# Performance work log

Hardware: AMD Instinct MI355X
Metric: run time of the kernel (lower is better)

## Reference

```python
import jax, jax.numpy as jnp
import numpy as np

EPS = 1e-15
BALL_EPS = 4e-3   # geoopt float32 projection eps
N_DST = 20000
N_EDGE = 200000
DIM = 128
H, D = 2, 128


def _norm(x):
    return jnp.sqrt(jnp.maximum(jnp.sum(x * x, -1, keepdims=True), EPS * EPS))


def _artanh(x):
    return jnp.arctanh(jnp.clip(x, -1.0 + 1e-7, 1.0 - 1e-7))


def mobius_add(x, y):
    x2 = jnp.sum(x * x, -1, keepdims=True)
    y2 = jnp.sum(y * y, -1, keepdims=True)
    xy = jnp.sum(x * y, -1, keepdims=True)
    num = (1 + 2 * xy + y2) * x + (1 - x2) * y
    den = 1 + 2 * xy + x2 * y2
    return num / jnp.maximum(den, EPS)


def mobius_matvec(W, x):
    xn = _norm(x)
    mx = x @ W.T
    mxn = _norm(mx)
    return jnp.tanh(mxn / xn * _artanh(xn)) * mx / mxn


def logmap0(y):
    yn = _norm(y)
    return _artanh(yn) * y / yn


def expmap0(u):
    un = _norm(u)
    return jnp.tanh(un) * u / un


def projx(x):
    n = _norm(x)
    maxn = 1.0 - BALL_EPS
    return jnp.where(n > maxn, x * (maxn / n), x)


def ball_dist(x, y):
    # dist(x,y) = 2 artanh(|| (-x) (+) y ||)
    return 2.0 * _artanh(_norm(mobius_add(-x, y))[..., 0])


def edge_softmax(logits, dst, n_dst):
    # softmax over edges grouped by destination node, per trailing dims
    m = jax.ops.segment_max(logits, dst, num_segments=n_dst)
    z = jnp.exp(logits - m[dst])
    s = jax.ops.segment_sum(z, dst, num_segments=n_dst)
    return z / s[dst]


def setup_inputs() -> dict:
    key = jax.random.key(0)
    ks = jax.random.split(key, 8)
    hyper = expmap0(0.2 * jax.random.normal(ks[0], (N_DST + N_EDGE, DIM), jnp.float32))
    dt = jax.random.uniform(ks[1], (N_EDGE,), jnp.float32) * 1e4
    time_w = jnp.asarray(1.0 / 10 ** np.linspace(0, 9, DIM, dtype=np.float32))
    time_b = jnp.zeros((DIM,), jnp.float32)
    w_src = 0.05 * jax.random.normal(ks[2], (H * D, DIM), jnp.float32)
    b_src = 0.01 * jax.random.normal(ks[3], (H * D,), jnp.float32)
    w_dst = 0.05 * jax.random.normal(ks[4], (H * D, DIM), jnp.float32)
    b_dst = 0.01 * jax.random.normal(ks[5], (H * D,), jnp.float32)
    attn = 0.1 * jax.random.normal(ks[6], (1, H, D), jnp.float32)
    src_idx = jnp.arange(N_EDGE, dtype=jnp.int32) + N_DST  # edge i's src node
    dst_idx = jax.random.randint(ks[7], (N_EDGE,), 0, N_DST, jnp.int32)
    return {"hyper": hyper, "dt": dt, "time_w": time_w, "time_b": time_b,
            "w_src": w_src, "b_src": b_src, "w_dst": w_dst, "b_dst": b_dst,
            "attn": attn, "src_idx": src_idx, "dst_idx": dst_idx}


def reference(hyper, dt, time_w, time_b, w_src, b_src, w_dst, b_dst, attn, src_idx, dst_idx):
    n_dst = N_DST
    # time encoding: zeros for dst nodes, dt for the sampled neighbor of each edge
    time = jnp.concatenate([jnp.zeros((n_dst,), dt.dtype), dt])        # [num_src]
    time_feat = jnp.cos(time[:, None] * time_w[None, :] + time_b)      # [num_src, DIM]
    time_feat = projx(time_feat)
    src_feat = mobius_add(hyper, time_feat)                            # [num_src, DIM]
    h_dst = src_feat[:n_dst]
    feat_src = mobius_add(mobius_matvec(w_src, src_feat), b_src)       # [num_src, H*D]
    feat_dst = mobius_add(mobius_matvec(w_dst, h_dst), b_dst)          # [n_dst, H*D]
    el = logmap0(feat_src).reshape(-1, H, D)
    er = logmap0(feat_dst).reshape(-1, H, D)
    # attention logit per edge/head
    e = jnp.sum((el[src_idx] + er[dst_idx]) * attn, -1)[:, :, None]    # [E,H,1]
    # hyperbolic-distance gate, edge-softmax normalized
    d = ball_dist(feat_src[src_idx], feat_dst[dst_idx])                # [E]
    inv = 1.0 / (1e-15 + d)
    dsm = edge_softmax(inv[:, None], dst_idx, n_dst)[:, :, None]       # [E,1,1]
    e = jax.nn.leaky_relu(e * dsm, 0.2)
    a = edge_softmax(e, dst_idx, n_dst)                                # [E,H,1]
    ft = jax.ops.segment_sum(el[src_idx] * a, dst_idx, num_segments=n_dst)
    rst = ft.reshape(n_dst, H * D)
    return expmap0(rst)
```

## Files before the change

kernel.cpp:

```cpp
#include <hip/hip_runtime.h>
#include <hip/hip_bf16.h>
#include <math.h>

typedef __attribute__((ext_vector_type(8))) short bfrag8;
typedef __attribute__((ext_vector_type(4))) float ffrag4;

__device__ inline float bf2f(unsigned short h) { return __uint_as_float(((unsigned)h) << 16); }
__device__ inline unsigned short f2bf(float f) {
    unsigned u = __float_as_uint(f);
    unsigned r = (u + 0x7FFFu + ((u >> 16) & 1u)) >> 16;
    return (unsigned short)r;
}
__device__ inline float wred(float v) {
    v += __shfl_xor(v, 1, 64);
    v += __shfl_xor(v, 2, 64);
    v += __shfl_xor(v, 4, 64);
    v += __shfl_xor(v, 8, 64);
    v += __shfl_xor(v, 16, 64);
    v += __shfl_xor(v, 32, 64);
    return v;
}
__device__ inline float wredmax(float v) {
    v = fmaxf(v, __shfl_xor(v, 1, 64));
    v = fmaxf(v, __shfl_xor(v, 2, 64));
    v = fmaxf(v, __shfl_xor(v, 4, 64));
    v = fmaxf(v, __shfl_xor(v, 8, 64));
    v = fmaxf(v, __shfl_xor(v, 16, 64));
    v = fmaxf(v, __shfl_xor(v, 32, 64));
    return v;
}
__device__ inline float bsum(float v, float* red) {
    v = wred(v);
    if ((threadIdx.x & 63) == 0) red[threadIdx.x >> 6] = v;
    __syncthreads();
    float r = red[0] + red[1] + red[2] + red[3];
    __syncthreads();
    return r;
}

#define ACLIP (1.0f - 1e-7f)

__global__ void k_detect(const unsigned short* __restrict__ hyper, int* __restrict__ flag) {
    __shared__ int total;
    int t = threadIdx.x;
    if (t == 0) total = 0;
    __syncthreads();
    int cnt = 0;
    for (int i = t * 8; i < t * 8 + 8; i++) {
        if ((i & 1) == 0) {
            unsigned e = ((unsigned)hyper[i] >> 7) & 0xFF;
            if (e >= 0xC0) cnt++;
        }
    }
    atomicAdd(&total, cnt);
    __syncthreads();
    if (t == 0) *flag = (total >= 32) ? 1 : 0;
}

__device__ inline float ldin(const void* s, int i, int isf32) {
    return isf32 ? ((const float*)s)[i] : bf2f(((const unsigned short*)s)[i]);
}
__global__ void k_params(const void* __restrict__ w_src, const void* __restrict__ w_dst,
                         const void* __restrict__ b_src, const void* __restrict__ b_dst,
                         const void* __restrict__ attn, const void* __restrict__ time_w,
                         const void* __restrict__ time_b,
                         unsigned short* __restrict__ whs, unsigned short* __restrict__ wls,
                         unsigned short* __restrict__ whd, unsigned short* __restrict__ wld,
                         float* __restrict__ bsrc, float* __restrict__ bdst,
                         float* __restrict__ pattn, float* __restrict__ tw,
                         float* __restrict__ tb, const int* __restrict__ flag, int nw) {
    int i = blockIdx.x * blockDim.x + threadIdx.x;
    int isf32 = *flag;
    if (i < nw) {
        float x = ldin(w_src, i, isf32);
        unsigned short h = f2bf(x);
        whs[i] = h; wls[i] = f2bf(x - bf2f(h));
        float y = ldin(w_dst, i, isf32);
        unsigned short g = f2bf(y);
        whd[i] = g; wld[i] = f2bf(y - bf2f(g));
    }
    if (i < 256) {
        bsrc[i] = ldin(b_src, i, isf32);
        bdst[i] = ldin(b_dst, i, isf32);
        pattn[i] = ldin(attn, i, isf32);
    }
    if (i < 128) {
        tw[i] = ldin(time_w, i, isf32);
        tb[i] = ldin(time_b, i, isf32);
    }
}
__global__ void k_fill(unsigned* __restrict__ p, unsigned v, int n) {
    int i = blockIdx.x * blockDim.x + threadIdx.x;
    if (i < n) p[i] = v;
}

__global__ void k_hist(const int* __restrict__ dst_idx, int* __restrict__ deg, int n_edge) {
    int i = blockIdx.x * blockDim.x + threadIdx.x;
    if (i < n_edge) atomicAdd(deg + dst_idx[i], 1);
}
__global__ __launch_bounds__(1024) void k_scan(const int* __restrict__ deg,
                                               int* __restrict__ rowptr,
                                               int* __restrict__ cursor, int n) {
    __shared__ int part[1024];
    int t = threadIdx.x;
    int chunk = (n + 1023) >> 10;
    int lo = t * chunk, hi = min(lo + chunk, n);
    int s = 0;
    for (int i = lo; i < hi; i++) s += deg[i];
    part[t] = s;
    __syncthreads();
    for (int dd = 1; dd < 1024; dd <<= 1) {
        int v = (t >= dd) ? part[t - dd] : 0;
        __syncthreads();
        part[t] += v;
        __syncthreads();
    }
    int base = (t == 0) ? 0 : part[t - 1];
    for (int i = lo; i < hi; i++) {
        rowptr[i] = base; cursor[i] = base;
        base += deg[i];
    }
    if (t == 0) rowptr[n] = part[1023];
}
__global__ void k_scatter_edges(const int* __restrict__ src_idx, const int* __restrict__ dst_idx,
                                int* __restrict__ cursor, int* __restrict__ es, int n_edge) {
    int i = blockIdx.x * blockDim.x + threadIdx.x;
    if (i >= n_edge) return;
    int slot = atomicAdd(cursor + dst_idx[i], 1);
    es[slot] = src_idx[i];
}

__global__ void k_node_prep(const void* __restrict__ hyper_v,
                            const void* __restrict__ dt_v,
                            const float* __restrict__ tw, const float* __restrict__ tb,
                            unsigned short* __restrict__ Ah, unsigned short* __restrict__ Al,
                            float* __restrict__ tnode,
                            const int* __restrict__ flag, int n_dst, int n_total) {
    int wid  = (blockIdx.x * blockDim.x + threadIdx.x) >> 6;
    int lane = threadIdx.x & 63;
    if (wid >= n_total) return;
    int isf32 = *flag;
    float tval = 0.0f;
    if (wid >= n_dst) {
        int e = wid - n_dst;
        tval = isf32 ? ((const float*)dt_v)[e] : bf2f(((const unsigned short*)dt_v)[e]);
    }
    int j0 = lane * 2;
    float tf0 = cosf(tval * tw[j0]     + tb[j0]);
    float tf1 = cosf(tval * tw[j0 + 1] + tb[j0 + 1]);
    float h0, h1;
    if (isf32) {
        const float* hp = (const float*)hyper_v + (size_t)wid * 128 + j0;
        h0 = hp[0]; h1 = hp[1];
    } else {
        const unsigned short* hp = (const unsigned short*)hyper_v + (size_t)wid * 128 + j0;
        h0 = bf2f(hp[0]); h1 = bf2f(hp[1]);
    }
    float ptf2 = wred(tf0 * tf0 + tf1 * tf1);
    float ph2  = wred(h0 * h0 + h1 * h1);
    float pht  = wred(h0 * tf0 + h1 * tf1);
    float ntf = sqrtf(fmaxf(ptf2, 1e-30f));
    float maxn = 1.0f - 0.004f;
    float sc = (ntf > maxn) ? (maxn / ntf) : 1.0f;
    float y2 = sc * sc * ptf2, xy = sc * pht, x2 = ph2;
    float A = 1.0f + 2.0f * xy + y2;
    float B = 1.0f - x2;
    float iden = 1.0f / fmaxf(1.0f + 2.0f * xy + x2 * y2, 1e-15f);
    float s0 = (A * h0 + B * sc * tf0) * iden;
    float s1 = (A * h1 + B * sc * tf1) * iden;
    unsigned short h0s = f2bf(s0), h1s = f2bf(s1);
    unsigned short l0s = f2bf(s0 - bf2f(h0s)), l1s = f2bf(s1 - bf2f(h1s));
    *(ushort2*)(Ah + (size_t)wid * 128 + j0) = make_ushort2(h0s, h1s);
    *(ushort2*)(Al + (size_t)wid * 128 + j0) = make_ushort2(l0s, l1s);
    float ps2 = wred(s0 * s0 + s1 * s1);
    float xn = sqrtf(fmaxf(ps2, 1e-30f));
    float g = atanhf(fminf(xn, ACLIP)) / xn;
    if (lane == 0) tnode[wid] = g;
}

#define WPITCH 136
#define GEMM_LDS (256 * WPITCH * 2 * 2)
__global__ __launch_bounds__(512, 2) void k_gemm_ep(
        const unsigned short* __restrict__ Ah, const unsigned short* __restrict__ Al,
        const unsigned short* __restrict__ Wh, const unsigned short* __restrict__ Wl,
        const float* __restrict__ bvec, const float* __restrict__ attn,
        const float* __restrict__ tnode,
        float* __restrict__ feat, float* __restrict__ x2a, float* __restrict__ ca,
        float* __restrict__ satt, int base, int M) {
    extern __shared__ unsigned short smem[];
    unsigned short* Bhs = smem;
    unsigned short* Bls = smem + 256 * WPITCH;

    int t = threadIdx.x;
    for (int v = t; v < 4096; v += 512) {
        int e = v << 3;
        int row = e >> 7, col = e & 127;
        *(bfrag8*)(Bhs + row * WPITCH + col) = *(const bfrag8*)(Wh + e);
        *(bfrag8*)(Bls + row * WPITCH + col) = *(const bfrag8*)(Wl + e);
    }
    __syncthreads();

    int w = t >> 6, lane = t & 63;
    int m16 = lane & 15, kg = lane >> 4;
    int rowbase = (blockIdx.x * 8 + w) * 32;
    int ar0 = min(rowbase + m16, M - 1);
    int ar1 = min(rowbase + 16 + m16, M - 1);
    const unsigned short* A0h = Ah + (size_t)ar0 * 128;
    const unsigned short* A0l = Al + (size_t)ar0 * 128;
    const unsigned short* A1h = Ah + (size_t)ar1 * 128;
    const unsigned short* A1l = Al + (size_t)ar1 * 128;

    ffrag4 acc[2][16];
#pragma unroll
    for (int p = 0; p < 2; p++)
#pragma unroll
        for (int ct = 0; ct < 16; ct++) acc[p][ct] = (ffrag4){0.0f, 0.0f, 0.0f, 0.0f};

    int kA = kg * 8;
    bfrag8 ah0 = *(const bfrag8*)(A0h + kA);
    bfrag8 al0 = *(const bfrag8*)(A0l + kA);
    bfrag8 ah1 = *(const bfrag8*)(A1h + kA);
    bfrag8 al1 = *(const bfrag8*)(A1l + kA);

    for (int ks = 0; ks < 4; ks++) {
        bfrag8 nh0 = ah0, nl0 = al0, nh1 = ah1, nl1 = al1;
        if (ks < 3) {
            int kn = (ks + 1) * 32 + kA;
            nh0 = *(const bfrag8*)(A0h + kn);
            nl0 = *(const bfrag8*)(A0l + kn);
            nh1 = *(const bfrag8*)(A1h + kn);
            nl1 = *(const bfrag8*)(A1l + kn);
        }
        int k0 = ks * 32 + kA;
#pragma unroll
        for (int ct = 0; ct < 16; ct++) {
            int wb = (ct * 16 + m16) * WPITCH + k0;
            bfrag8 bh = *(const bfrag8*)(Bhs + wb);
            bfrag8 bl = *(const bfrag8*)(Bls + wb);
            acc[0][ct] = __builtin_amdgcn_mfma_f32_16x16x32_bf16(ah0, bh, acc[0][ct], 0, 0, 0);
            acc[0][ct] = __builtin_amdgcn_mfma_f32_16x16x32_bf16(al0, bh, acc[0][ct], 0, 0, 0);
            acc[0][ct] = __builtin_amdgcn_mfma_f32_16x16x32_bf16(ah0, bl, acc[0][ct], 0, 0, 0);
            acc[1][ct] = __builtin_amdgcn_mfma_f32_16x16x32_bf16(ah1, bh, acc[1][ct], 0, 0, 0);
            acc[1][ct] = __builtin_amdgcn_mfma_f32_16x16x32_bf16(al1, bh, acc[1][ct], 0, 0, 0);
            acc[1][ct] = __builtin_amdgcn_mfma_f32_16x16x32_bf16(ah1, bl, acc[1][ct], 0, 0, 0);
        }
        ah0 = nh0; al0 = nl0; ah1 = nh1; al1 = nl1;
    }

    float bv[16], av[16];
    float pb2 = 0.0f;
#pragma unroll
    for (int ct = 0; ct < 16; ct++) {
        bv[ct] = bvec[ct * 16 + m16];
        av[ct] = attn[ct * 16 + m16];
        pb2 += bv[ct] * bv[ct];
    }
#pragma unroll
    for (int off = 1; off < 16; off <<= 1) pb2 += __shfl_xor(pb2, off, 64);

#pragma unroll
    for (int p = 0; p < 2; p++) {
        float pm2[4] = {0, 0, 0, 0}, pdb[4] = {0, 0, 0, 0};
#pragma unroll
        for (int ct = 0; ct < 16; ct++)
#pragma unroll
            for (int r = 0; r < 4; r++) {
                float v = acc[p][ct][r];
                pm2[r] += v * v;
                pdb[r] += v * bv[ct];
            }
#pragma unroll
        for (int off = 1; off < 16; off <<= 1)
#pragma unroll
            for (int r = 0; r < 4; r++) {
                pm2[r] += __shfl_xor(pm2[r], off, 64);
                pdb[r] += __shfl_xor(pdb[r], off, 64);
            }
#pragma unroll
        for (int r = 0; r < 4; r++) {
            int row_o = rowbase + p * 16 + kg * 4 + r;
            bool ok = row_o < M;
            float g = ok ? tnode[base + row_o] : 1.0f;
            float mxn = sqrtf(fmaxf(pm2[r], 1e-30f));
            float sv = tanhf(mxn * g) / mxn;
            float xy = sv * pdb[r];
            float x2v = sv * sv * pm2[r];
            float Am = 1.0f + 2.0f * xy + pb2;
            float Bm = 1.0f - x2v;
            float iden = 1.0f / fmaxf(1.0f + 2.0f * xy + x2v * pb2, 1e-15f);
            float pf2 = 0.0f, pa0 = 0.0f, pa1 = 0.0f;
#pragma unroll
            for (int ct = 0; ct < 16; ct++) {
                float f = (Am * sv * acc[p][ct][r] + Bm * bv[ct]) * iden;
                acc[p][ct][r] = f;
                pf2 += f * f;
                if (ct < 8) pa0 += f * av[ct]; else pa1 += f * av[ct];
            }
#pragma unroll
            for (int off = 1; off < 16; off <<= 1) {
                pf2 += __shfl_xor(pf2, off, 64);
                pa0 += __shfl_xor(pa0, off, 64);
                pa1 += __shfl_xor(pa1, off, 64);
            }
            if (ok) {
                float* fr = feat + (size_t)(base + row_o) * 256;
#pragma unroll
                for (int ct = 0; ct < 16; ct++) fr[ct * 16 + m16] = acc[p][ct][r];
                if (m16 == 0) {
                    float nf = sqrtf(fmaxf(pf2, 1e-30f));
                    float cl = atanhf(fminf(nf, ACLIP)) / nf;
                    x2a[base + row_o] = pf2;
                    ca[base + row_o] = cl;
                    satt[(size_t)(base + row_o) * 2 + 0] = cl * pa0;
                    satt[(size_t)(base + row_o) * 2 + 1] = cl * pa1;
                }
            }
        }
    }
}

#define CAPR 16
#define CAPE 64
__global__ __launch_bounds__(256) void k_aggregate(
        const int* __restrict__ rowptr, const int* __restrict__ es,
        const float* __restrict__ x2a, const float* __restrict__ satt,
        const float* __restrict__ ca, const float* __restrict__ feat,
        float* __restrict__ invg, float* __restrict__ w0g, float* __restrict__ w1g,
        void* __restrict__ out, const int* __restrict__ flag, int n_dst) {
    __shared__ float red[4];
    __shared__ float yrow[256];
    __shared__ float inv_s[CAPE], w0_s[CAPE], w1_s[CAPE];
    __shared__ int sb_s[CAPE];
    __shared__ float cache[CAPR * 256];
    int d = blockIdx.x;
    int t = threadIdx.x;
    int w = t >> 6, lane = t & 63;
    int off0 = rowptr[d], off1 = rowptr[d + 1];
    int deg = off1 - off0;
    if (deg == 0) {
        if (*flag) ((float*)out)[(size_t)d * 256 + t] = 0.0f;
        else ((unsigned short*)out)[(size_t)d * 256 + t] = 0;
        return;
    }
    yrow[t] = feat[(size_t)d * 256 + t];
    float y2 = x2a[d];
    __syncthreads();

    int c = lane * 4;
    float4 yv = *(const float4*)(&yrow[c]);
    for (int b = 0; b < deg; b += 4) {
        int j = b + w;
        if (j < deg) {
            int i = off0 + j;
            int s = es[i];
            float4 xv = *(const float4*)(feat + (size_t)s * 256 + c);
            float pd = wred(xv.x * yv.x + xv.y * yv.y + xv.z * yv.z + xv.w * yv.w);
            if (j < CAPR) *(float4*)&cache[j * 256 + c] = xv;
            if (lane == 0) {
                float x2 = x2a[s];
                float A = 1.0f - 2.0f * pd + y2;
                float B = 1.0f - x2;
                float iden = 1.0f / fmaxf(1.0f - 2.0f * pd + x2 * y2, 1e-15f);
                float p2 = fmaxf(A * A * x2 - 2.0f * A * B * pd + B * B * y2, 0.0f);
                float nrm = sqrtf(fmaxf(p2, 1e-30f)) * iden;
                float dd = 2.0f * atanhf(fminf(nrm, ACLIP));
                float iv = 1.0f / (1e-15f + dd);
                if (j < CAPE) { inv_s[j] = iv; sb_s[j] = s; }
                else { invg[i] = iv; }
            }
        }
    }
    __syncthreads();

    if (w == 0) {
        float sd0 = satt[(size_t)d * 2 + 0], sd1 = satt[(size_t)d * 2 + 1];
        float lm = -INFINITY;
        for (int j = lane; j < deg; j += 64)
            lm = fmaxf(lm, (j < CAPE) ? inv_s[j] : invg[off0 + j]);
        float m1 = wredmax(lm);
        float ls = 0.0f;
        for (int j = lane; j < deg; j += 64)
            ls += expf(((j < CAPE) ? inv_s[j] : invg[off0 + j]) - m1);
        float is1 = 1.0f / wred(ls);
        float lm0 = -INFINITY, lm1 = -INFINITY;
        for (int j = lane; j < deg; j += 64) {
            int s = (j < CAPE) ? sb_s[j] : es[off0 + j];
            float iv = (j < CAPE) ? inv_s[j] : invg[off0 + j];
            float dsm = expf(iv - m1) * is1;
            float e0 = (satt[(size_t)s * 2 + 0] + sd0) * dsm; e0 = (e0 > 0.0f) ? e0 : 0.2f * e0;
            float e1 = (satt[(size_t)s * 2 + 1] + sd1) * dsm; e1 = (e1 > 0.0f) ? e1 : 0.2f * e1;
            if (j < CAPE) { w0_s[j] = e0; w1_s[j] = e1; }
            else { w0g[off0 + j] = e0; w1g[off0 + j] = e1; }
            lm0 = fmaxf(lm0, e0); lm1 = fmaxf(lm1, e1);
        }
        float m20 = wredmax(lm0), m21 = wredmax(lm1);
        float l20 = 0.0f, l21 = 0.0f;
        for (int j = lane; j < deg; j += 64) {
            float e0 = (j < CAPE) ? w0_s[j] : w0g[off0 + j];
            float e1 = (j < CAPE) ? w1_s[j] : w1g[off0 + j];
            l20 += expf(e0 - m20); l21 += expf(e1 - m21);
        }
        float is20 = 1.0f / wred(l20), is21 = 1.0f / wred(l21);
        for (int j = lane; j < deg; j += 64) {
            int s = (j < CAPE) ? sb_s[j] : es[off0 + j];
            float cs = ca[s];
            if (j < CAPE) {
                w0_s[j] = expf(w0_s[j] - m20) * is20 * cs;
                w1_s[j] = expf(w1_s[j] - m21) * is21 * cs;
            } else {
                w0g[off0 + j] = expf(w0g[off0 + j] - m20) * is20 * cs;
                w1g[off0 + j] = expf(w1g[off0 + j] - m21) * is21 * cs;
            }
        }
    }
    __syncthreads();

    int col = t, h = t >> 7;
    float acc = 0.0f;
    for (int j = 0; j < deg; j++) {
        float wgt = (j < CAPE) ? (h ? w1_s[j] : w0_s[j])
                               : (h ? w1g[off0 + j] : w0g[off0 + j]);
        float x;
        if (j < CAPR) x = cache[j * 256 + col];
        else {
            int s = (j < CAPE) ? sb_s[j] : es[off0 + j];
            x = feat[(size_t)s * 256 + col];
        }
        acc += wgt * x;
    }
    float p2 = bsum(acc * acc, red);
    float n = sqrtf(fmaxf(p2, 1e-30f));
    float sc = tanhf(n) / n;
    float o = acc * sc;
    if (*flag) ((float*)out)[(size_t)d * 256 + col] = o;
    else ((unsigned short*)out)[(size_t)d * 256 + col] = f2bf(o);
}

extern "C" void kernel_launch(void* const* d_in, const int* in_sizes, int n_in,
                              void* d_out, int out_size, void* d_ws, size_t ws_size,
                              hipStream_t stream) {
    const void* hyper  = d_in[0];
    const void* dt     = d_in[1];
    const void* time_w = d_in[2];
    const void* time_b = d_in[3];
    const void* w_src  = d_in[4];
    const void* b_src  = d_in[5];
    const void* w_dst  = d_in[6];
    const void* b_dst  = d_in[7];
    const void* attn   = d_in[8];
    const int* src_idx = (const int*)d_in[9];
    const int* dst_idx = (const int*)d_in[10];

    const int DIMN = 128, HD = 256;
    int n_edge  = in_sizes[1];
    int n_total = in_sizes[0] / DIMN;
    int n_dst   = n_total - n_edge;

    float* ws = (float*)d_ws;
    size_t off = 0;
    auto alloc = [&](size_t n) { float* p = ws + off; off += n; return p; };
    float* p_tw    = alloc(DIMN);
    float* p_tb    = alloc(DIMN);
    float* p_bsrc  = alloc(HD);
    float* p_bdst  = alloc(HD);
    float* p_attn  = alloc(HD);
    int*   p_flag  = (int*)alloc(4);
    unsigned short* p_whs = (unsigned short*)alloc((size_t)HD * DIMN / 2);
    unsigned short* p_wls = (unsigned short*)alloc((size_t)HD * DIMN / 2);
    unsigned short* p_whd = (unsigned short*)alloc((size_t)HD * DIMN / 2);
    unsigned short* p_wld = (unsigned short*)alloc((size_t)HD * DIMN / 2);
    unsigned short* p_ah = (unsigned short*)alloc((size_t)n_total * DIMN / 2);
    unsigned short* p_al = (unsigned short*)alloc((size_t)n_total * DIMN / 2);
    int* p_deg    = (int*)alloc(n_dst);
    int* p_rowptr = (int*)alloc(n_dst + 1);
    int* p_cursor = (int*)alloc(n_dst);
    int* p_es     = (int*)alloc(n_edge);
    float* p_inv  = alloc(n_edge);
    float* p_w0   = alloc(n_edge);
    float* p_w1   = alloc(n_edge);
    float* p_feat  = alloc((size_t)n_total * HD);
    float* p_tnode = alloc(n_total);
    float* p_call  = alloc(n_total);
    float* p_x2    = alloc(n_total);
    float* p_satt  = alloc((size_t)n_total * 2);
    (void)ws_size;

    const int TB = 256;
    auto cdiv = [](int a, int b) { return (a + b - 1) / b; };

    static bool lds_cfg = false;
    if (!lds_cfg) {
        hipFuncSetAttribute(reinterpret_cast<const void*>(k_gemm_ep),
                            hipFuncAttributeMaxDynamicSharedMemorySize, GEMM_LDS);
        lds_cfg = true;
    }

    k_detect<<<1, TB, 0, stream>>>((const unsigned short*)hyper, p_flag);

    k_params<<<cdiv(HD * DIMN, TB), TB, 0, stream>>>(
        w_src, w_dst, b_src, b_dst, attn, time_w, time_b,
        p_whs, p_wls, p_whd, p_wld, p_bsrc, p_bdst, p_attn, p_tw, p_tb,
        p_flag, HD * DIMN);

    k_fill<<<cdiv(n_dst, TB), TB, 0, stream>>>((unsigned*)p_deg, 0u, n_dst);
    k_hist<<<cdiv(n_edge, TB), TB, 0, stream>>>(dst_idx, p_deg, n_edge);
    k_scan<<<1, 1024, 0, stream>>>(p_deg, p_rowptr, p_cursor, n_dst);
    k_scatter_edges<<<cdiv(n_edge, TB), TB, 0, stream>>>(src_idx, dst_idx, p_cursor,
                                                         p_es, n_edge);

    k_node_prep<<<cdiv(n_total, 4), TB, 0, stream>>>(hyper, dt, p_tw, p_tb,
                                                     p_ah, p_al, p_tnode, p_flag,
                                                     n_dst, n_total);

    k_gemm_ep<<<cdiv(n_dst, 256), 512, GEMM_LDS, stream>>>(p_ah, p_al, p_whd, p_wld,
                                                           p_bdst, p_attn, p_tnode,
                                                           p_feat, p_x2, p_call, p_satt,
                                                           0, n_dst);
    k_gemm_ep<<<cdiv(n_edge, 256), 512, GEMM_LDS, stream>>>(p_ah + (size_t)n_dst * DIMN,
                                                            p_al + (size_t)n_dst * DIMN,
                                                            p_whs, p_wls,
                                                            p_bsrc, p_attn, p_tnode,
                                                            p_feat, p_x2, p_call, p_satt,
                                                            n_dst, n_edge);

    k_aggregate<<<n_dst, TB, 0, stream>>>(p_rowptr, p_es, p_x2, p_satt, p_call,
                                          p_feat, p_inv, p_w0, p_w1,
                                          d_out, p_flag, n_dst);
}
```

Before: 594.8 us.

## Use fast transcendentals, remap edge distance loop, add single-pass softmax path

```diff
diff --git a/kernel.cpp b/kernel.cpp
--- a/kernel.cpp
+++ b/kernel.cpp
@@ -39,6 +39,36 @@
 }
 
 #define ACLIP (1.0f - 1e-7f)
+#define ATANH_ACLIP 8.4056196f
+
+__device__ inline float rcpf(float x) { return __builtin_amdgcn_rcpf(x); }
+__device__ inline float fsqrtf(float x) { return __builtin_amdgcn_sqrtf(x); }
+__device__ inline float fexp(float x) { return __expf(x); }
+__device__ inline float flog(float x) { return __logf(x); }
+__device__ inline float atanh_over_x(float x) {
+    if (x < 0.125f) {
+        float x2 = x * x;
+        return 1.0f + x2 * (0.33333333f + x2 * 0.2f);
+    }
+    return 0.5f * flog((1.0f + x) * rcpf(1.0f - x)) * rcpf(x);
+}
+__device__ inline float tanh_over_x(float x) {
+    if (x < 0.125f) {
+        float x2 = x * x;
+        return 1.0f - x2 * (0.33333333f - x2 * 0.13333333f);
+    }
+    float e = fexp(-2.0f * x);
+    return (1.0f - e) * rcpf((1.0f + e) * x);
+}
+__device__ inline float fcosr(float x) {
+    const float C  = 0.15915494309189535f;
+    const float C1 = 0.1591796875f;
+    const float C2 = -2.4744408e-5f;
+    float k = __builtin_rintf(x * C);
+    float f = fmaf(x, C1, -k);
+    f = fmaf(x, C2, f);
+    return __builtin_amdgcn_cosf(f);
+}
 
 __global__ void k_detect(const unsigned short* __restrict__ hyper, int* __restrict__ flag) {
     __shared__ int total;
@@ -146,8 +176,8 @@
         tval = isf32 ? ((const float*)dt_v)[e] : bf2f(((const unsigned short*)dt_v)[e]);
     }
     int j0 = lane * 2;
-    float tf0 = cosf(tval * tw[j0]     + tb[j0]);
-    float tf1 = cosf(tval * tw[j0 + 1] + tb[j0 + 1]);
+    float tf0 = fcosr(tval * tw[j0]     + tb[j0]);
+    float tf1 = fcosr(tval * tw[j0 + 1] + tb[j0 + 1]);
     float h0, h1;
     if (isf32) {
         const float* hp = (const float*)hyper_v + (size_t)wid * 128 + j0;
@@ -159,13 +189,13 @@
     float ptf2 = wred(tf0 * tf0 + tf1 * tf1);
     float ph2  = wred(h0 * h0 + h1 * h1);
     float pht  = wred(h0 * tf0 + h1 * tf1);
-    float ntf = sqrtf(fmaxf(ptf2, 1e-30f));
+    float ntf = fsqrtf(fmaxf(ptf2, 1e-30f));
     float maxn = 1.0f - 0.004f;
-    float sc = (ntf > maxn) ? (maxn / ntf) : 1.0f;
+    float sc = (ntf > maxn) ? (maxn * rcpf(ntf)) : 1.0f;
     float y2 = sc * sc * ptf2, xy = sc * pht, x2 = ph2;
     float A = 1.0f + 2.0f * xy + y2;
     float B = 1.0f - x2;
-    float iden = 1.0f / fmaxf(1.0f + 2.0f * xy + x2 * y2, 1e-15f);
+    float iden = rcpf(fmaxf(1.0f + 2.0f * xy + x2 * y2, 1e-15f));
     float s0 = (A * h0 + B * sc * tf0) * iden;
     float s1 = (A * h1 + B * sc * tf1) * iden;
     unsigned short h0s = f2bf(s0), h1s = f2bf(s1);
@@ -173,8 +203,8 @@
     *(ushort2*)(Ah + (size_t)wid * 128 + j0) = make_ushort2(h0s, h1s);
     *(ushort2*)(Al + (size_t)wid * 128 + j0) = make_ushort2(l0s, l1s);
     float ps2 = wred(s0 * s0 + s1 * s1);
-    float xn = sqrtf(fmaxf(ps2, 1e-30f));
-    float g = atanhf(fminf(xn, ACLIP)) / xn;
+    float xn = fsqrtf(fmaxf(ps2, 1e-30f));
+    float g = (xn > ACLIP) ? (ATANH_ACLIP * rcpf(xn)) : atanh_over_x(xn);
     if (lane == 0) tnode[wid] = g;
 }
 
@@ -281,13 +311,13 @@
             int row_o = rowbase + p * 16 + kg * 4 + r;
             bool ok = row_o < M;
             float g = ok ? tnode[base + row_o] : 1.0f;
-            float mxn = sqrtf(fmaxf(pm2[r], 1e-30f));
-            float sv = tanhf(mxn * g) / mxn;
+            float mxn = fsqrtf(fmaxf(pm2[r], 1e-30f));
+            float sv = g * tanh_over_x(mxn * g);
             float xy = sv * pdb[r];
             float x2v = sv * sv * pm2[r];
             float Am = 1.0f + 2.0f * xy + pb2;
             float Bm = 1.0f - x2v;
-            float iden = 1.0f / fmaxf(1.0f + 2.0f * xy + x2v * pb2, 1e-15f);
+            float iden = rcpf(fmaxf(1.0f + 2.0f * xy + x2v * pb2, 1e-15f));
             float pf2 = 0.0f, pa0 = 0.0f, pa1 = 0.0f;
 #pragma unroll
             for (int ct = 0; ct < 16; ct++) {
@@ -307,8 +337,8 @@
 #pragma unroll
                 for (int ct = 0; ct < 16; ct++) fr[ct * 16 + m16] = acc[p][ct][r];
                 if (m16 == 0) {
-                    float nf = sqrtf(fmaxf(pf2, 1e-30f));
-                    float cl = atanhf(fminf(nf, ACLIP)) / nf;
+                    float nf = fsqrtf(fmaxf(pf2, 1e-30f));
+                    float cl = (nf > ACLIP) ? (ATANH_ACLIP * rcpf(nf)) : atanh_over_x(nf);
                     x2a[base + row_o] = pf2;
                     ca[base + row_o] = cl;
                     satt[(size_t)(base + row_o) * 2 + 0] = cl * pa0;
@@ -346,25 +376,47 @@
     float y2 = x2a[d];
     __syncthreads();
 
-    int c = lane * 4;
-    float4 yv = *(const float4*)(&yrow[c]);
-    for (int b = 0; b < deg; b += 4) {
-        int j = b + w;
+    int g16 = lane >> 4, sub = lane & 15;
+    int cb = sub * 16;
+    float4 yv0 = *(const float4*)(&yrow[cb + 0]);
+    float4 yv1 = *(const float4*)(&yrow[cb + 4]);
+    float4 yv2 = *(const float4*)(&yrow[cb + 8]);
+    float4 yv3 = *(const float4*)(&yrow[cb + 12]);
+    for (int b = 0; b < deg; b += 16) {
+        int j = b + w * 4 + g16;
         if (j < deg) {
             int i = off0 + j;
             int s = es[i];
-            float4 xv = *(const float4*)(feat + (size_t)s * 256 + c);
-            float pd = wred(xv.x * yv.x + xv.y * yv.y + xv.z * yv.z + xv.w * yv.w);
-            if (j < CAPR) *(float4*)&cache[j * 256 + c] = xv;
-            if (lane == 0) {
+            const float* xr = feat + (size_t)s * 256 + cb;
+            float4 x0 = *(const float4*)(xr + 0);
+            float4 x1 = *(const float4*)(xr + 4);
+            float4 x2f = *(const float4*)(xr + 8);
+            float4 x3 = *(const float4*)(xr + 12);
+            float pd = x0.x * yv0.x + x0.y * yv0.y + x0.z * yv0.z + x0.w * yv0.w
+                     + x1.x * yv1.x + x1.y * yv1.y + x1.z * yv1.z + x1.w * yv1.w
+                     + x2f.x * yv2.x + x2f.y * yv2.y + x2f.z * yv2.z + x2f.w * yv2.w
+                     + x3.x * yv3.x + x3.y * yv3.y + x3.z * yv3.z + x3.w * yv3.w;
+            pd += __shfl_xor(pd, 1, 64);
+            pd += __shfl_xor(pd, 2, 64);
+            pd += __shfl_xor(pd, 4, 64);
+            pd += __shfl_xor(pd, 8, 64);
+            if (j < CAPR) {
+                float* cr = &cache[j * 256 + cb];
+                *(float4*)(cr + 0) = x0;
+                *(float4*)(cr + 4) = x1;
+                *(float4*)(cr + 8) = x2f;
+                *(float4*)(cr + 12) = x3;
+            }
+            if (sub == 0) {
                 float x2 = x2a[s];
                 float A = 1.0f - 2.0f * pd + y2;
                 float B = 1.0f - x2;
-                float iden = 1.0f / fmaxf(1.0f - 2.0f * pd + x2 * y2, 1e-15f);
+                float iden = rcpf(fmaxf(1.0f - 2.0f * pd + x2 * y2, 1e-15f));
                 float p2 = fmaxf(A * A * x2 - 2.0f * A * B * pd + B * B * y2, 0.0f);
-                float nrm = sqrtf(fmaxf(p2, 1e-30f)) * iden;
-                float dd = 2.0f * atanhf(fminf(nrm, ACLIP));
-                float iv = 1.0f / (1e-15f + dd);
+                float nrm = fsqrtf(fmaxf(p2, 1e-30f)) * iden;
+                float xc = fminf(nrm, ACLIP);
+                float dd = 2.0f * xc * atanh_over_x(xc);
+                float iv = rcpf(1e-15f + dd);
                 if (j < CAPE) { inv_s[j] = iv; sb_s[j] = s; }
                 else { invg[i] = iv; }
             }
@@ -374,42 +426,68 @@
 
     if (w == 0) {
         float sd0 = satt[(size_t)d * 2 + 0], sd1 = satt[(size_t)d * 2 + 1];
-        float lm = -INFINITY;
-        for (int j = lane; j < deg; j += 64)
-            lm = fmaxf(lm, (j < CAPE) ? inv_s[j] : invg[off0 + j]);
-        float m1 = wredmax(lm);
-        float ls = 0.0f;
-        for (int j = lane; j < deg; j += 64)
-            ls += expf(((j < CAPE) ? inv_s[j] : invg[off0 + j]) - m1);
-        float is1 = 1.0f / wred(ls);
-        float lm0 = -INFINITY, lm1 = -INFINITY;
-        for (int j = lane; j < deg; j += 64) {
-            int s = (j < CAPE) ? sb_s[j] : es[off0 + j];
-            float iv = (j < CAPE) ? inv_s[j] : invg[off0 + j];
-            float dsm = expf(iv - m1) * is1;
-            float e0 = (satt[(size_t)s * 2 + 0] + sd0) * dsm; e0 = (e0 > 0.0f) ? e0 : 0.2f * e0;
-            float e1 = (satt[(size_t)s * 2 + 1] + sd1) * dsm; e1 = (e1 > 0.0f) ? e1 : 0.2f * e1;
-            if (j < CAPE) { w0_s[j] = e0; w1_s[j] = e1; }
-            else { w0g[off0 + j] = e0; w1g[off0 + j] = e1; }
-            lm0 = fmaxf(lm0, e0); lm1 = fmaxf(lm1, e1);
-        }
-        float m20 = wredmax(lm0), m21 = wredmax(lm1);
-        float l20 = 0.0f, l21 = 0.0f;
-        for (int j = lane; j < deg; j += 64) {
-            float e0 = (j < CAPE) ? w0_s[j] : w0g[off0 + j];
-            float e1 = (j < CAPE) ? w1_s[j] : w1g[off0 + j];
-            l20 += expf(e0 - m20); l21 += expf(e1 - m21);
-        }
-        float is20 = 1.0f / wred(l20), is21 = 1.0f / wred(l21);
-        for (int j = lane; j < deg; j += 64) {
-            int s = (j < CAPE) ? sb_s[j] : es[off0 + j];
-            float cs = ca[s];
-            if (j < CAPE) {
-                w0_s[j] = expf(w0_s[j] - m20) * is20 * cs;
-                w1_s[j] = expf(w1_s[j] - m21) * is21 * cs;
-            } else {
-                w0g[off0 + j] = expf(w0g[off0 + j] - m20) * is20 * cs;
-                w1g[off0 + j] = expf(w1g[off0 + j] - m21) * is21 * cs;
+        if (deg <= CAPE) {
+            int j = lane;
+            bool act = j < deg;
+            int s = act ? sb_s[j] : 0;
+            float iv = act ? inv_s[j] : -INFINITY;
+            float m1 = wredmax(iv);
+            float z = fexp(iv - m1);
+            float is1 = rcpf(wred(z));
+            float dsm = z * is1;
+            float a0 = act ? satt[(size_t)s * 2 + 0] : 0.0f;
+            float a1 = act ? satt[(size_t)s * 2 + 1] : 0.0f;
+            float e0 = (a0 + sd0) * dsm; e0 = (e0 > 0.0f) ? e0 : 0.2f * e0;
+            float e1 = (a1 + sd1) * dsm; e1 = (e1 > 0.0f) ? e1 : 0.2f * e1;
+            float m20 = wredmax(act ? e0 : -INFINITY);
+            float m21 = wredmax(act ? e1 : -INFINITY);
+            float z0 = act ? fexp(e0 - m20) : 0.0f;
+            float z1 = act ? fexp(e1 - m21) : 0.0f;
+            float is20 = rcpf(wred(z0));
+            float is21 = rcpf(wred(z1));
+            if (act) {
+                float cs = ca[s];
+                w0_s[j] = z0 * is20 * cs;
+                w1_s[j] = z1 * is21 * cs;
+            }
+        } else {
+            float lm = -INFINITY;
+            for (int j = lane; j < deg; j += 64)
+                lm = fmaxf(lm, (j < CAPE) ? inv_s[j] : invg[off0 + j]);
+            float m1 = wredmax(lm);
+            float ls = 0.0f;
+            for (int j = lane; j < deg; j += 64)
+                ls += fexp(((j < CAPE) ? inv_s[j] : invg[off0 + j]) - m1);
+            float is1 = rcpf(wred(ls));
+            float lm0 = -INFINITY, lm1 = -INFINITY;
+            for (int j = lane; j < deg; j += 64) {
+                int s = (j < CAPE) ? sb_s[j] : es[off0 + j];
+                float iv = (j < CAPE) ? inv_s[j] : invg[off0 + j];
+                float dsm = fexp(iv - m1) * is1;
+                float e0 = (satt[(size_t)s * 2 + 0] + sd0) * dsm; e0 = (e0 > 0.0f) ? e0 : 0.2f * e0;
+                float e1 = (satt[(size_t)s * 2 + 1] + sd1) * dsm; e1 = (e1 > 0.0f) ? e1 : 0.2f * e1;
+                if (j < CAPE) { w0_s[j] = e0; w1_s[j] = e1; }
+                else { w0g[off0 + j] = e0; w1g[off0 + j] = e1; }
+                lm0 = fmaxf(lm0, e0); lm1 = fmaxf(lm1, e1);
+            }
+            float m20 = wredmax(lm0), m21 = wredmax(lm1);
+            float l20 = 0.0f, l21 = 0.0f;
+            for (int j = lane; j < deg; j += 64) {
+                float e0 = (j < CAPE) ? w0_s[j] : w0g[off0 + j];
+                float e1 = (j < CAPE) ? w1_s[j] : w1g[off0 + j];
+                l20 += fexp(e0 - m20); l21 += fexp(e1 - m21);
+            }
+            float is20 = rcpf(wred(l20)), is21 = rcpf(wred(l21));
+            for (int j = lane; j < deg; j += 64) {
+                int s = (j < CAPE) ? sb_s[j] : es[off0 + j];
+                float cs = ca[s];
+                if (j < CAPE) {
+                    w0_s[j] = fexp(w0_s[j] - m20) * is20 * cs;
+                    w1_s[j] = fexp(w1_s[j] - m21) * is21 * cs;
+                } else {
+                    w0g[off0 + j] = fexp(w0g[off0 + j] - m20) * is20 * cs;
+                    w1g[off0 + j] = fexp(w1g[off0 + j] - m21) * is21 * cs;
+                }
             }
         }
     }
@@ -429,8 +507,8 @@
         acc += wgt * x;
     }
     float p2 = bsum(acc * acc, red);
-    float n = sqrtf(fmaxf(p2, 1e-30f));
-    float sc = tanhf(n) / n;
+    float n = fsqrtf(fmaxf(p2, 1e-30f));
+    float sc = tanh_over_x(n);
     float o = acc * sc;
     if (*flag) ((float*)out)[(size_t)d * 256 + col] = o;
     else ((unsigned short*)out)[(size_t)d * 256 + col] = f2bf(o);
```

Result: faster. 507.9 us (-14.6%).
